# Performance work log

Measured on AMD Instinct MI355X. Metric: run time of the kernel, lower is better.

## Reference

```python
import jax, jax.numpy as jnp
import numpy as np
from math import sqrt

L, H, D, HD, F, V, P = 8, 16, 1024, 64, 4096, 32000, 2048
B, S = 2, 2048
EPS = 1e-5


def _ln(x, g, b):
    m = jnp.mean(x, axis=-1, keepdims=True)
    v = jnp.mean((x - m) ** 2, axis=-1, keepdims=True)
    return (x - m) * jax.lax.rsqrt(v + EPS) * g + b


def setup_inputs() -> dict:
    key = jax.random.key(0)
    ks = jax.random.split(key, 12)
    w = 0.02
    return {
        'input_ids': jax.random.randint(ks[0], (B, S), 0, V),
        'tok_emb': jax.random.normal(ks[1], (V, D), jnp.float32) * w,
        'pos_emb': jax.random.normal(ks[2], (P, D), jnp.float32) * w,
        'emb_g': jnp.ones((D,), jnp.float32),
        'emb_b': jnp.zeros((D,), jnp.float32),
        'ln1_g': jnp.ones((L, D), jnp.float32),
        'ln1_b': jnp.zeros((L, D), jnp.float32),
        'ln2_g': jnp.ones((L, D), jnp.float32),
        'ln2_b': jnp.zeros((L, D), jnp.float32),
        'Wq': jax.random.normal(ks[3], (L, H, D, HD), jnp.float32) * w,
        'bq': jnp.zeros((L, H, HD), jnp.float32),
        'Wk': jax.random.normal(ks[4], (L, H, D, HD), jnp.float32) * w,
        'bk': jnp.zeros((L, H, HD), jnp.float32),
        'Wv': jax.random.normal(ks[5], (L, H, D, HD), jnp.float32) * w,
        'bv': jnp.zeros((L, H, HD), jnp.float32),
        'Wo': jax.random.normal(ks[6], (L, D, D), jnp.float32) * w,
        'bo': jnp.zeros((L, D), jnp.float32),
        'W1': jax.random.normal(ks[7], (L, D, F), jnp.float32) * w,
        'b1': jnp.zeros((L, F), jnp.float32),
        'W2': jax.random.normal(ks[8], (L, F, D), jnp.float32) * w,
        'b2': jnp.zeros((L, D), jnp.float32),
    }


def _encoder(input_ids, tok_emb, pos_emb, emb_g, emb_b, ln1_g, ln1_b, ln2_g,
             ln2_b, Wq, bq, Wk, bk, Wv, bv, Wo, bo, W1, b1, W2, b2):
    seq = input_ids.shape[-1]
    x = tok_emb[input_ids] + pos_emb[:seq][None, :, :]  # [B,S,D]
    x = _ln(x, emb_g, emb_b)  # dropout = identity (eval)

    scale = 1.0 / sqrt(HD)

    def layer(x, p):
        (g1, b1_, g2, b2_, wq, bq_, wk, bk_, wv, bv_, wo, bo_, w1, bb1, w2, bb2) = p
        h = _ln(x, g1, b1_)
        q = jnp.einsum('bsd,hdk->bhsk', h, wq) + bq_[:, None, :]
        k = jnp.einsum('bsd,hdk->bhsk', h, wk) + bk_[:, None, :]
        v = jnp.einsum('bsd,hdk->bhsk', h, wv) + bv_[:, None, :]
        scores = jnp.einsum('bhsk,bhtk->bhst', q, k) * scale
        w = jax.nn.softmax(scores, axis=-1)
        av = jnp.einsum('bhst,bhtk->bhsk', w, v)  # [B,H,S,hd]
        av = jnp.transpose(av, (0, 2, 1, 3)).reshape(x.shape[0], x.shape[1], D)
        x = x + jnp.einsum('bsd,de->bse', av, wo) + bo_
        h2 = _ln(x, g2, b2_)
        f = jax.nn.gelu(jnp.einsum('bsd,df->bsf', h2, w1) + bb1, approximate=False)
        x = x + jnp.einsum('bsf,fd->bsd', f, w2) + bb2
        return x, None

    xs = (ln1_g, ln1_b, ln2_g, ln2_b, Wq, bq, Wk, bk, Wv, bv, Wo, bo, W1, b1, W2, b2)
    x, _ = jax.lax.scan(layer, x, xs)
    return x


def reference(input_ids, tok_emb, pos_emb, emb_g, emb_b, ln1_g, ln1_b, ln2_g,
              ln2_b, Wq, bq, Wk, bk, Wv, bv, Wo, bo, W1, b1, W2, b2):
    return _encoder(input_ids, tok_emb, pos_emb, emb_g, emb_b, ln1_g, ln1_b,
                    ln2_g, ln2_b, Wq, bq, Wk, bk, Wv, bv, Wo, bo, W1, b1, W2, b2)
```

## Files before the change

### kernel.cpp

```cpp
#include <hip/hip_runtime.h>
#include <hip/hip_bf16.h>

#define L_ 8
#define H_ 16
#define D_ 1024
#define HD_ 64
#define F_ 4096
#define B_ 2
#define S_ 2048
#define NTOK (B_*S_)

typedef unsigned short u16;
typedef __bf16 bf16x8 __attribute__((ext_vector_type(8)));
typedef float f32x4 __attribute__((ext_vector_type(4)));

__device__ __forceinline__ u16 f2b(float f){ union{float f; unsigned u;} c; c.f = f; unsigned u = c.u; return (u16)((u + 0x7fffu + ((u>>16)&1u)) >> 16); }
__device__ __forceinline__ u16 f2b_fast(float f){ union{float f; unsigned u;} c; c.f = f; return (u16)((c.u + 0x8000u) >> 16); }
__device__ __forceinline__ float b2f(u16 x){ union{unsigned u; float f;} c; c.u = ((unsigned)x)<<16; return c.f; }

__device__ __forceinline__ void gload16(const u16* g, u16* l){
  __builtin_amdgcn_global_load_lds(
      (const __attribute__((address_space(1))) void*)g,
      (__attribute__((address_space(3))) void*)l,
      16 , 0 , 0 );
}

#define WAITV_BAR(n) do { \
  asm volatile("s_waitcnt vmcnt(%0)" :: "i"(n) : "memory"); \
  __builtin_amdgcn_sched_barrier(0); \
  __builtin_amdgcn_s_barrier(); \
} while(0)

__device__ __forceinline__ void blk_reduce2(float& a, float& b, float* sm){
  for (int off=32; off>0; off>>=1){ a += __shfl_down(a,off); b += __shfl_down(b,off); }
  int w = threadIdx.x>>6, ln = threadIdx.x&63;
  if (ln==0){ sm[w]=a; sm[4+w]=b; }
  __syncthreads();
  a = sm[0]+sm[1]+sm[2]+sm[3];
  b = sm[4]+sm[5]+sm[6]+sm[7];
}

__global__ __launch_bounds__(256) void embed_ln(const int* __restrict__ ids,
    const float* __restrict__ tok, const float* __restrict__ pos,
    const float* __restrict__ g, const float* __restrict__ bb,
    float* __restrict__ x)
{
  __shared__ float sm[8];
  int row = blockIdx.x;
  int s   = row % S_;
  int id  = ids[row];
  const float* te = tok + (size_t)id * D_;
  const float* pe = pos + (size_t)s  * D_;
  float v[4]; float sum=0.f, sq=0.f;
  #pragma unroll
  for (int i=0;i<4;i++){ int d = threadIdx.x + i*256; v[i] = te[d] + pe[d]; sum += v[i]; sq += v[i]*v[i]; }
  blk_reduce2(sum, sq, sm);
  float mean = sum * (1.0f/D_);
  float var  = sq  * (1.0f/D_) - mean*mean;
  float inv  = rsqrtf(var + 1e-5f);
  #pragma unroll
  for (int i=0;i<4;i++){ int d = threadIdx.x + i*256; x[(size_t)row*D_ + d] = (v[i]-mean)*inv*g[d] + bb[d]; }
}

__global__ __launch_bounds__(256) void ln_f32_bf16(const float* __restrict__ x,
    const float* __restrict__ g, const float* __restrict__ bb, u16* __restrict__ out)
{
  __shared__ float sm[8];
  int row = blockIdx.x;
  const float* xr = x + (size_t)row*D_;
  float v[4]; float sum=0.f, sq=0.f;
  #pragma unroll
  for (int i=0;i<4;i++){ int d = threadIdx.x + i*256; v[i] = xr[d]; sum += v[i]; sq += v[i]*v[i]; }
  blk_reduce2(sum, sq, sm);
  float mean = sum * (1.0f/D_);
  float var  = sq  * (1.0f/D_) - mean*mean;
  float inv  = rsqrtf(var + 1e-5f);
  #pragma unroll
  for (int i=0;i<4;i++){ int d = threadIdx.x + i*256; out[(size_t)row*D_ + d] = f2b((v[i]-mean)*inv*g[d] + bb[d]); }
}

__global__ __launch_bounds__(256) void transpose_w(const float* __restrict__ src,
    u16* __restrict__ dst, int R, int C)
{
  __shared__ u16 tile[32][33];
  int c0 = blockIdx.x*32, r0 = blockIdx.y*32;
  int tx = threadIdx.x, ty = threadIdx.y;
  #pragma unroll
  for (int i=0;i<4;i++){
    int r = ty + i*8;
    tile[r][tx] = f2b(src[(size_t)(r0+r)*C + c0 + tx]);
  }
  __syncthreads();
  #pragma unroll
  for (int i=0;i<4;i++){
    int c = ty + i*8;
    dst[(size_t)(c0+c)*R + r0 + tx] = tile[tx][c];
  }
}

__global__ __launch_bounds__(256) void qkv_repack(const float* __restrict__ Wq,
    const float* __restrict__ Wk, const float* __restrict__ Wv,
    u16* __restrict__ dst, int layer)
{
  __shared__ u16 tile[32][33];
  int z = blockIdx.z; int which = z >> 4, h = z & 15;
  const float* W = (which==0) ? Wq : (which==1) ? Wk : Wv;
  const float* src = W + ((size_t)(layer*H_ + h))*D_*HD_;
  int d0 = blockIdx.x*32, c0 = blockIdx.y*32;
  int tx = threadIdx.x, ty = threadIdx.y;
  #pragma unroll
  for (int i=0;i<4;i++){
    int r = ty + i*8;
    tile[r][tx] = f2b(src[(size_t)(d0+r)*HD_ + c0 + tx]);
  }
  __syncthreads();
  #pragma unroll
  for (int i=0;i<4;i++){
    int hd = c0 + ty + i*8;
    dst[(size_t)(which*1024 + h*64 + hd)*D_ + d0 + tx] = tile[tx][ty + i*8];
  }
}

__global__ __launch_bounds__(256) void v_transpose(const u16* __restrict__ qkv, u16* __restrict__ vT)
{
  __shared__ u16 tile[64*64];
  const int tt = blockIdx.x;
  const int bh = blockIdx.y;
  const int b = bh>>4, h = bh&15;
  const int t = threadIdx.x;
  const u16* src = qkv + (size_t)(b*S_ + tt*64)*3072 + 2048 + h*64;
  #pragma unroll
  for (int i=0;i<2;i++){
    int idx = t + i*256;
    int tl = idx>>3, hc = idx&7;
    uint4 v = *(const uint4*)(src + (size_t)tl*3072 + hc*8);
    *(uint4*)(&tile[tl*64 + ((hc ^ (tl&7))<<3)]) = v;
  }
  __syncthreads();
  u16* dst = vT + ((size_t)bh*64)*S_ + tt*64;
  #pragma unroll
  for (int i=0;i<2;i++){
    int idx = t + i*256;
    int hd = idx>>3, tc = idx&7;
    u16 tmp[8];
    #pragma unroll
    for (int j=0;j<8;j++){
      int tk = tc*8 + j;
      tmp[j] = tile[tk*64 + (hd ^ ((tk&7)<<3))];
    }
    *(uint4*)(dst + (size_t)hd*S_ + tc*8) = *(uint4*)tmp;
  }
}

__device__ __forceinline__ void epi_store(float v0,float v1,float v2,float v3,
    float* xres, u16* obf, size_t idx, int epi)
{
  if (epi==1){
    float4 t = *(float4*)(xres + idx);
    t.x += v0; t.y += v1; t.z += v2; t.w += v3;
    *(float4*)(xres + idx) = t;
  } else {
    if (epi==2){
      #define GELU_T(v) { float t2=(v)*(v); float u=(v)*fmaf(t2,0.044715f,1.0f); \
                          float e=exp2f(u*-2.3022082f); (v)=(v)*__builtin_amdgcn_rcpf(1.0f+e); }
      GELU_T(v0); GELU_T(v1); GELU_T(v2); GELU_T(v3);
      #undef GELU_T
    }
    uint2 w;
    w.x = (unsigned)f2b_fast(v0) | ((unsigned)f2b_fast(v1) << 16);
    w.y = (unsigned)f2b_fast(v2) | ((unsigned)f2b_fast(v3) << 16);
    *(uint2*)(obf + idx) = w;
  }
}

__global__ __launch_bounds__(256) void gemm_bf16(
    const u16* __restrict__ A, const u16* __restrict__ Bt,
    const float* __restrict__ bias0, const float* __restrict__ bias1, const float* __restrict__ bias2,
    float* __restrict__ xres, u16* __restrict__ obf,
    int M, int N, int K, int epi)
{
  __shared__ u16 As[128*64];
  __shared__ u16 Bs[128*64];
  const int tid = threadIdx.x;
  const int nbx = gridDim.x;
  const int nwg = nbx * gridDim.y;
  int bid = blockIdx.x + nbx*blockIdx.y;
  int nid = (bid & 7)*(nwg >> 3) + (bid >> 3);
  const int bm = (nid % nbx) * 128;
  const int bn = (nid / nbx) * 128;
  const int wv = tid>>6, ln = tid&63;
  const int wr = wv>>1, wc = wv&1;
  const int l15 = ln&15, lhi = ln>>4;
  const int l8 = ln>>3;
  const int c8s = (ln&7) ^ l8;
  f32x4 acc[4][4];
  const f32x4 zero4 = {0.f,0.f,0.f,0.f};
  #pragma unroll
  for (int i=0;i<4;i++)
    #pragma unroll
    for (int j=0;j<4;j++) acc[i][j] = zero4;

  for (int k0 = 0; k0 < K; k0 += 64) {
    #pragma unroll
    for (int i=0;i<4;i++){
      int row = wv*8 + i*32 + l8;
      gload16(A  + (size_t)(bm+row)*K + k0 + c8s*8, &As[(wv*8 + i*32)*64]);
      gload16(Bt + (size_t)(bn+row)*K + k0 + c8s*8, &Bs[(wv*8 + i*32)*64]);
    }
    __syncthreads();
    #pragma unroll
    for (int ks=0; ks<2; ks++){
      bf16x8 af[4], bfr[4];
      #pragma unroll
      for (int i=0;i<4;i++){
        int ra = wr*64 + i*16 + l15;
        af[i]  = *(const bf16x8*)(&As[ra*64 + (((ks*4+lhi) ^ (ra&7))<<3)]);
        int rb = wc*64 + i*16 + l15;
        bfr[i] = *(const bf16x8*)(&Bs[rb*64 + (((ks*4+lhi) ^ (rb&7))<<3)]);
      }
      #pragma unroll
      for (int i=0;i<4;i++)
        #pragma unroll
        for (int j=0;j<4;j++)
          acc[i][j] = __builtin_amdgcn_mfma_f32_16x16x32_bf16(bfr[j], af[i], acc[i][j], 0,0,0);
    }
    __syncthreads();
  }

  #pragma unroll
  for (int j=0;j<4;j++){
    int col0 = bn + wc*64 + j*16 + lhi*4;
    float4 bv4;
    if (bias1){
      const float* bp = (col0 < 1024) ? (bias0 + col0)
                      : (col0 < 2048) ? (bias1 + col0 - 1024)
                                      : (bias2 + col0 - 2048);
      bv4 = *(const float4*)bp;
    } else {
      bv4 = *(const float4*)(bias0 + col0);
    }
    #pragma unroll
    for (int i=0;i<4;i++){
      int row = bm + wr*64 + i*16 + l15;
      epi_store(acc[i][j][0]+bv4.x, acc[i][j][1]+bv4.y, acc[i][j][2]+bv4.z, acc[i][j][3]+bv4.w,
                xres, obf, (size_t)row*N + col0, epi);
    }
  }
}

__global__ __launch_bounds__(512,2) void gemm256(
    const u16* __restrict__ A, const u16* __restrict__ Bt,
    const float* __restrict__ bias0, const float* __restrict__ bias1, const float* __restrict__ bias2,
    float* __restrict__ xres, u16* __restrict__ obf,
    int M, int N, int K, int epi)
{
  __shared__ u16 As[2][256*64];
  __shared__ u16 Bs[2][256*64];
  const int tid = threadIdx.x;
  const int nbx = gridDim.x;
  const int nwg = nbx * gridDim.y;
  int bid = blockIdx.x + nbx*blockIdx.y;
  int nid = (bid & 7)*(nwg >> 3) + (bid >> 3);
  const int bm = (nid % nbx) * 256;
  const int bn = (nid / nbx) * 256;
  const int wv = tid>>6, ln = tid&63;
  const int wm = wv>>2, wn = wv&3;
  const int l15 = ln&15, lhi = ln>>4;
  const int l8 = ln>>3;
  const int c8s = (ln&7) ^ l8;

  f32x4 acc[2][2][4][2];
  const f32x4 zero4 = {0.f,0.f,0.f,0.f};
  #pragma unroll
  for (int a=0;a<2;a++)
    #pragma unroll
    for (int b=0;b<2;b++)
      #pragma unroll
      for (int i=0;i<4;i++)
        #pragma unroll
        for (int j=0;j<2;j++) acc[a][b][i][j] = zero4;

  const u16* aB0 = A  + (size_t)(bm + wv*16 + l8)*K + c8s*8;
  const u16* bB0 = Bt + (size_t)(bn + wv*16 + l8)*K + c8s*8;

  #define ISSUE(c, kt) do {                                                  \
    const u16* aB = aB0 + (size_t)(kt)*64;                                   \
    const u16* bB = bB0 + (size_t)(kt)*64;                                   \
    gload16(aB,                 &As[c][(wv*16      )*64]);                   \
    gload16(aB + (size_t)8*K,   &As[c][(wv*16 +   8)*64]);                   \
    gload16(bB,                 &Bs[c][(wv*16      )*64]);                   \
    gload16(bB + (size_t)8*K,   &Bs[c][(wv*16 +   8)*64]);                   \
    gload16(bB + (size_t)128*K, &Bs[c][(128 + wv*16    )*64]);               \
    gload16(bB + (size_t)136*K, &Bs[c][(128 + wv*16 + 8)*64]);               \
    gload16(aB + (size_t)128*K, &As[c][(128 + wv*16    )*64]);               \
    gload16(aB + (size_t)136*K, &As[c][(128 + wv*16 + 8)*64]);               \
  } while(0)

  #define READ_B(c) do {                                                     \
    _Pragma("unroll")                                                        \
    for (int qc=0;qc<2;qc++)                                                 \
      _Pragma("unroll")                                                      \
      for (int j=0;j<2;j++){                                                 \
        int rb = qc*128 + wn*32 + j*16 + l15;                                \
        _Pragma("unroll")                                                    \
        for (int ks=0;ks<2;ks++)                                             \
          bfr[qc][j][ks] = *(const bf16x8*)(&Bs[c][rb*64 + (((ks*4+lhi) ^ (rb&7))<<3)]); \
      }                                                                      \
  } while(0)

  #define READ_A(c, qr) do {                                                 \
    _Pragma("unroll")                                                        \
    for (int i=0;i<4;i++){                                                   \
      int ra = (qr)*128 + wm*64 + i*16 + l15;                                \
      _Pragma("unroll")                                                      \
      for (int ks=0;ks<2;ks++)                                               \
        af[i][ks] = *(const bf16x8*)(&As[c][ra*64 + (((ks*4+lhi) ^ (ra&7))<<3)]); \
    }                                                                        \
  } while(0)

  #define MFMA_Q(qr) do {                                                    \
    __builtin_amdgcn_s_setprio(1);                                           \
    _Pragma("unroll")                                                        \
    for (int ks=0;ks<2;ks++)                                                 \
      _Pragma("unroll")                                                      \
      for (int i=0;i<4;i++)                                                  \
        _Pragma("unroll")                                                    \
        for (int qc=0;qc<2;qc++)                                             \
          _Pragma("unroll")                                                  \
          for (int j=0;j<2;j++)                                              \
            acc[qr][qc][i][j] = __builtin_amdgcn_mfma_f32_16x16x32_bf16(     \
                bfr[qc][j][ks], af[i][ks], acc[qr][qc][i][j], 0,0,0);        \
    __builtin_amdgcn_s_setprio(0);                                           \
  } while(0)

  const int nt = K >> 6;
  ISSUE(0, 0);
  WAITV_BAR(2);
  for (int t=0; t<nt-1; ++t){
    int c = t&1;
    ISSUE(c^1, t+1);
    bf16x8 bfr[2][2][2], af[4][2];
    READ_B(c);
    READ_A(c, 0);
    MFMA_Q(0);
    WAITV_BAR(8);
    READ_A(c, 1);
    MFMA_Q(1);
    WAITV_BAR(2);
  }
  {
    int c = (nt-1)&1;
    bf16x8 bfr[2][2][2], af[4][2];
    READ_B(c);
    READ_A(c, 0);
    MFMA_Q(0);
    WAITV_BAR(0);
    READ_A(c, 1);
    MFMA_Q(1);
  }
  #undef ISSUE
  #undef READ_B
  #undef READ_A
  #undef MFMA_Q

  #pragma unroll
  for (int qc=0; qc<2; qc++)
    #pragma unroll
    for (int j=0;j<2;j++){
      int col0 = bn + qc*128 + wn*32 + j*16 + lhi*4;
      float4 bv4;
      if (bias1){
        const float* bp = (col0 < 1024) ? (bias0 + col0)
                        : (col0 < 2048) ? (bias1 + col0 - 1024)
                                        : (bias2 + col0 - 2048);
        bv4 = *(const float4*)bp;
      } else {
        bv4 = *(const float4*)(bias0 + col0);
      }
      #pragma unroll
      for (int qr=0; qr<2; qr++)
        #pragma unroll
        for (int i=0;i<4;i++){
          int row = bm + qr*128 + wm*64 + i*16 + l15;
          epi_store(acc[qr][qc][i][j][0]+bv4.x, acc[qr][qc][i][j][1]+bv4.y,
                    acc[qr][qc][i][j][2]+bv4.z, acc[qr][qc][i][j][3]+bv4.w,
                    xres, obf, (size_t)row*N + col0, epi);
        }
    }
}

__global__ __launch_bounds__(256) void attn_fwd(const u16* __restrict__ qkv,
    const u16* __restrict__ vT, u16* __restrict__ att)
{
  __shared__ u16 Ks[2][64*64];
  __shared__ u16 Vs[2][64*64];
  const int tid = threadIdx.x, wv = tid>>6, ln = tid&63, l15 = ln&15, lhi = ln>>4;
  const int l8 = ln>>3;
  const int cs = (ln&7) ^ l8;
  int bid = blockIdx.x + 32*(blockIdx.y + 16*blockIdx.z);
  int nid = (bid & 7)*128 + (bid >> 3);
  const int qt = nid & 31, h = (nid >> 5) & 15, b = nid >> 9;
  const u16* qg = qkv + (size_t)b*S_*3072 + h*64;
  const u16* kg = qg + 1024;
  const u16* vtg = vT + ((size_t)(b*16 + h)*64)*S_;

  bf16x8 qf[2];
  {
    const u16* qrow = qg + (size_t)(qt*64 + wv*16 + l15)*3072;
    u16 tmp[16];
    *(uint4*)(tmp)   = *(const uint4*)(qrow + lhi*8);
    *(uint4*)(tmp+8) = *(const uint4*)(qrow + 32 + lhi*8);
    #pragma unroll
    for (int i=0;i<16;i++) tmp[i] = f2b_fast(b2f(tmp[i]) * 0.18033688f);
    qf[0] = *(const bf16x8*)(tmp);
    qf[1] = *(const bf16x8*)(tmp+8);
  }
  const f32x4 zero4 = {0.f,0.f,0.f,0.f};
  f32x4 oacc[4];
  #pragma unroll
  for (int j=0;j<4;j++) oacc[j] = zero4;
  float lsum = 0.f;

  #define STAGE_KV(bufi, kti) do {                                            \
    _Pragma("unroll")                                                         \
    for (int i_=0;i_<2;i_++){                                                 \
      int r0_ = wv*8 + i_*32;                                                 \
      int row_ = r0_ + l8;                                                    \
      gload16(kg  + (size_t)((kti)*64+row_)*3072 + cs*8, &Ks[bufi][r0_*64]);  \
      gload16(vtg + (size_t)row_*S_ + (kti)*64 + cs*8,   &Vs[bufi][r0_*64]);  \
    }                                                                         \
  } while(0)

  STAGE_KV(0, 0);
  __syncthreads();
  int buf = 0;

  for (int kt=0; kt<S_/64; kt++){
    if (kt+1 < S_/64) STAGE_KV(buf^1, kt+1);

    f32x4 s[4];
    __builtin_amdgcn_s_setprio(1);
    #pragma unroll
    for (int j=0;j<4;j++){
      s[j] = zero4;
      #pragma unroll
      for (int ks=0; ks<2; ks++){
        int kr = j*16 + l15;
        bf16x8 kf = *(const bf16x8*)(&Ks[buf][kr*64 + (((ks*4+lhi) ^ (kr&7))<<3)]);
        s[j] = __builtin_amdgcn_mfma_f32_16x16x32_bf16(kf, qf[ks], s[j], 0,0,0);
      }
    }
    __builtin_amdgcn_s_setprio(0);

    unsigned pk[8];
    float part = 0.f;
    #pragma unroll
    for (int j=0;j<4;j++){
      float p0 = exp2f(s[j][0]);
      float p1 = exp2f(s[j][1]);
      float p2 = exp2f(s[j][2]);
      float p3 = exp2f(s[j][3]);
      part += (p0+p1)+(p2+p3);
      asm("v_cvt_pk_bf16_f32 %0, %1, %2" : "=v"(pk[j*2])   : "v"(p0), "v"(p1));
      asm("v_cvt_pk_bf16_f32 %0, %1, %2" : "=v"(pk[j*2+1]) : "v"(p2), "v"(p3));
    }
    lsum += part;

    unsigned pw[2][4];
    #pragma unroll
    for (int ks=0; ks<2; ks++){
      #pragma unroll
      for (int w=0; w<4; w++){
        int src = l15 + (lhi&1)*32 + (w>>1)*16;
        unsigned a  = __shfl(pk[ks*4 + (w&1)],     src);
        unsigned bb = __shfl(pk[ks*4 + 2 + (w&1)], src);
        pw[ks][w] = (lhi & 2) ? bb : a;
      }
    }
    bf16x8 pf[2];
    #pragma unroll
    for (int ks=0; ks<2; ks++){
      union { unsigned u[4]; bf16x8 v; } pu;
      pu.u[0]=pw[ks][0]; pu.u[1]=pw[ks][1]; pu.u[2]=pw[ks][2]; pu.u[3]=pw[ks][3];
      pf[ks] = pu.v;
    }

    __builtin_amdgcn_s_setprio(1);
    #pragma unroll
    for (int dj=0; dj<4; dj++){
      #pragma unroll
      for (int ks=0; ks<2; ks++){
        int vr = dj*16 + l15;
        bf16x8 vf = *(const bf16x8*)(&Vs[buf][vr*64 + (((ks*4+lhi) ^ (vr&7))<<3)]);
        oacc[dj] = __builtin_amdgcn_mfma_f32_16x16x32_bf16(pf[ks], vf, oacc[dj], 0,0,0);
      }
    }
    __builtin_amdgcn_s_setprio(0);
    __syncthreads();
    buf ^= 1;
  }
  #undef STAGE_KV

  float tot = lsum + __shfl_xor(lsum, 16);
  tot += __shfl_xor(tot, 32);
  float inv[4];
  #pragma unroll
  for (int r=0;r<4;r++) inv[r] = __builtin_amdgcn_rcpf(__shfl(tot, lhi*4+r));

  #pragma unroll
  for (int dj=0; dj<4; dj++){
    #pragma unroll
    for (int r=0;r<4;r++){
      int q = lhi*4 + r;
      int token = qt*64 + wv*16 + q;
      att[(size_t)(b*S_ + token)*D_ + h*HD_ + dj*16 + l15] = f2b_fast(oacc[dj][r] * inv[r]);
    }
  }
}

extern "C" void kernel_launch(void* const* d_in, const int* in_sizes, int n_in,
                              void* d_out, int out_size, void* d_ws, size_t ws_size,
                              hipStream_t stream)
{
  const int*   ids   = (const int*)d_in[0];
  const float* tok   = (const float*)d_in[1];
  const float* pos   = (const float*)d_in[2];
  const float* emb_g = (const float*)d_in[3];
  const float* emb_b = (const float*)d_in[4];
  const float* ln1g  = (const float*)d_in[5];
  const float* ln1b  = (const float*)d_in[6];
  const float* ln2g  = (const float*)d_in[7];
  const float* ln2b  = (const float*)d_in[8];
  const float* Wq = (const float*)d_in[9];
  const float* bq = (const float*)d_in[10];
  const float* Wk = (const float*)d_in[11];
  const float* bk = (const float*)d_in[12];
  const float* Wv = (const float*)d_in[13];
  const float* bv = (const float*)d_in[14];
  const float* Wo = (const float*)d_in[15];
  const float* bo = (const float*)d_in[16];
  const float* W1 = (const float*)d_in[17];
  const float* b1 = (const float*)d_in[18];
  const float* W2 = (const float*)d_in[19];
  const float* b2 = (const float*)d_in[20];

  float* x = (float*)d_out;
  char* ws = (char*)d_ws;
  u16* h     = (u16*)(ws);
  u16* qkvb  = (u16*)(ws + 8388608);
  u16* att   = (u16*)(ws + 33554432);
  u16* fbuf  = (u16*)(ws + 41943040);
  u16* vT    = fbuf;
  u16* wqkvt = (u16*)(ws + 75497472);
  u16* wot   = (u16*)(ws + 81788928);
  u16* w1t   = (u16*)(ws + 83886080);
  u16* w2t   = (u16*)(ws + 92274688);

  embed_ln<<<NTOK, 256, 0, stream>>>(ids, tok, pos, emb_g, emb_b, x);

  for (int l=0; l<L_; l++){
    ln_f32_bf16<<<NTOK, 256, 0, stream>>>(x, ln1g + l*D_, ln1b + l*D_, h);
    qkv_repack<<<dim3(32,2,48), dim3(32,8), 0, stream>>>(Wq, Wk, Wv, wqkvt, l);
    gemm256<<<dim3(16,12), 512, 0, stream>>>(h, wqkvt,
        bq + l*1024, bk + l*1024, bv + l*1024,
        nullptr, qkvb, NTOK, 3072, 1024, 0);
    v_transpose<<<dim3(32,32), 256, 0, stream>>>(qkvb, vT);
    attn_fwd<<<dim3(S_/64, H_, B_), 256, 0, stream>>>(qkvb, vT, att);
    transpose_w<<<dim3(32,32), dim3(32,8), 0, stream>>>(Wo + (size_t)l*D_*D_, wot, D_, D_);
    gemm_bf16<<<dim3(32,8), 256, 0, stream>>>(att, wot,
        bo + l*D_, nullptr, nullptr,
        x, nullptr, NTOK, 1024, 1024, 1);
    ln_f32_bf16<<<NTOK, 256, 0, stream>>>(x, ln2g + l*D_, ln2b + l*D_, h);
    transpose_w<<<dim3(128,32), dim3(32,8), 0, stream>>>(W1 + (size_t)l*D_*F_, w1t, D_, F_);
    gemm256<<<dim3(16,16), 512, 0, stream>>>(h, w1t,
        b1 + l*F_, nullptr, nullptr,
        nullptr, fbuf, NTOK, 4096, 1024, 2);
    transpose_w<<<dim3(32,128), dim3(32,8), 0, stream>>>(W2 + (size_t)l*F_*D_, w2t, F_, D_);
    gemm_bf16<<<dim3(32,8), 256, 0, stream>>>(fbuf, w2t,
        b2 + l*D_, nullptr, nullptr,
        x, nullptr, NTOK, 1024, 4096, 1);
  }
}
```

Measured before the change: 2.441 ms.

## Process two query tiles per attention wave and vectorize layernorm loads

The attention kernel now handles 128 queries per block, with each wave computing two 16-row query tiles against the same staged K/V tile. Each K and V fragment read from LDS then feeds two MFMAs, and K/V global staging is halved per query. The cost is twice the accumulator registers, which may lower occupancy, and half as many blocks (512). The embedding and layernorm kernels also switch to float4 loads and packed stores.

```diff
diff --git a/kernel.cpp b/kernel.cpp
--- a/kernel.cpp
+++ b/kernel.cpp
@@ -49,17 +49,21 @@
   int row = blockIdx.x;
   int s   = row % S_;
   int id  = ids[row];
-  const float* te = tok + (size_t)id * D_;
-  const float* pe = pos + (size_t)s  * D_;
-  float v[4]; float sum=0.f, sq=0.f;
-  #pragma unroll
-  for (int i=0;i<4;i++){ int d = threadIdx.x + i*256; v[i] = te[d] + pe[d]; sum += v[i]; sq += v[i]*v[i]; }
+  int d0  = threadIdx.x*4;
+  float4 t4 = *(const float4*)(tok + (size_t)id*D_ + d0);
+  float4 p4 = *(const float4*)(pos + (size_t)s *D_ + d0);
+  float4 v; v.x=t4.x+p4.x; v.y=t4.y+p4.y; v.z=t4.z+p4.z; v.w=t4.w+p4.w;
+  float sum = (v.x+v.y)+(v.z+v.w);
+  float sq  = v.x*v.x+v.y*v.y+v.z*v.z+v.w*v.w;
   blk_reduce2(sum, sq, sm);
   float mean = sum * (1.0f/D_);
   float var  = sq  * (1.0f/D_) - mean*mean;
   float inv  = rsqrtf(var + 1e-5f);
-  #pragma unroll
-  for (int i=0;i<4;i++){ int d = threadIdx.x + i*256; x[(size_t)row*D_ + d] = (v[i]-mean)*inv*g[d] + bb[d]; }
+  float4 g4 = *(const float4*)(g + d0);
+  float4 b4 = *(const float4*)(bb + d0);
+  float4 o; o.x=(v.x-mean)*inv*g4.x+b4.x; o.y=(v.y-mean)*inv*g4.y+b4.y;
+            o.z=(v.z-mean)*inv*g4.z+b4.z; o.w=(v.w-mean)*inv*g4.w+b4.w;
+  *(float4*)(x + (size_t)row*D_ + d0) = o;
 }
 
 __global__ __launch_bounds__(256) void ln_f32_bf16(const float* __restrict__ x,
@@ -67,16 +71,20 @@
 {
   __shared__ float sm[8];
   int row = blockIdx.x;
-  const float* xr = x + (size_t)row*D_;
-  float v[4]; float sum=0.f, sq=0.f;
-  #pragma unroll
-  for (int i=0;i<4;i++){ int d = threadIdx.x + i*256; v[i] = xr[d]; sum += v[i]; sq += v[i]*v[i]; }
+  int d0  = threadIdx.x*4;
+  float4 v = *(const float4*)(x + (size_t)row*D_ + d0);
+  float sum = (v.x+v.y)+(v.z+v.w);
+  float sq  = v.x*v.x+v.y*v.y+v.z*v.z+v.w*v.w;
   blk_reduce2(sum, sq, sm);
   float mean = sum * (1.0f/D_);
   float var  = sq  * (1.0f/D_) - mean*mean;
   float inv  = rsqrtf(var + 1e-5f);
-  #pragma unroll
-  for (int i=0;i<4;i++){ int d = threadIdx.x + i*256; out[(size_t)row*D_ + d] = f2b((v[i]-mean)*inv*g[d] + bb[d]); }
+  float4 g4 = *(const float4*)(g + d0);
+  float4 b4 = *(const float4*)(bb + d0);
+  uint2 w;
+  w.x = (unsigned)f2b((v.x-mean)*inv*g4.x+b4.x) | ((unsigned)f2b((v.y-mean)*inv*g4.y+b4.y)<<16);
+  w.y = (unsigned)f2b((v.z-mean)*inv*g4.z+b4.z) | ((unsigned)f2b((v.w-mean)*inv*g4.w+b4.w)<<16);
+  *(uint2*)(out + (size_t)row*D_ + d0) = w;
 }
 
 __global__ __launch_bounds__(256) void transpose_w(const float* __restrict__ src,
@@ -397,29 +405,33 @@
   const int tid = threadIdx.x, wv = tid>>6, ln = tid&63, l15 = ln&15, lhi = ln>>4;
   const int l8 = ln>>3;
   const int cs = (ln&7) ^ l8;
-  int bid = blockIdx.x + 32*(blockIdx.y + 16*blockIdx.z);
-  int nid = (bid & 7)*128 + (bid >> 3);
-  const int qt = nid & 31, h = (nid >> 5) & 15, b = nid >> 9;
+  int bid = blockIdx.x + 16*(blockIdx.y + 16*blockIdx.z);
+  int nid = (bid & 7)*64 + (bid >> 3);
+  const int qt = nid & 15, h = (nid >> 4) & 15, b = nid >> 8;
   const u16* qg = qkv + (size_t)b*S_*3072 + h*64;
   const u16* kg = qg + 1024;
   const u16* vtg = vT + ((size_t)(b*16 + h)*64)*S_;
 
-  bf16x8 qf[2];
+  bf16x8 qfA[2], qfB[2];
   {
-    const u16* qrow = qg + (size_t)(qt*64 + wv*16 + l15)*3072;
-    u16 tmp[16];
-    *(uint4*)(tmp)   = *(const uint4*)(qrow + lhi*8);
-    *(uint4*)(tmp+8) = *(const uint4*)(qrow + 32 + lhi*8);
-    #pragma unroll
-    for (int i=0;i<16;i++) tmp[i] = f2b_fast(b2f(tmp[i]) * 0.18033688f);
-    qf[0] = *(const bf16x8*)(tmp);
-    qf[1] = *(const bf16x8*)(tmp+8);
+    const u16* qrA = qg + (size_t)(qt*128 + wv*32 + l15)*3072;
+    const u16* qrB = qrA + (size_t)16*3072;
+    u16 ta[16], tb[16];
+    *(uint4*)(ta)   = *(const uint4*)(qrA + lhi*8);
+    *(uint4*)(ta+8) = *(const uint4*)(qrA + 32 + lhi*8);
+    *(uint4*)(tb)   = *(const uint4*)(qrB + lhi*8);
+    *(uint4*)(tb+8) = *(const uint4*)(qrB + 32 + lhi*8);
+    #pragma unroll
+    for (int i=0;i<16;i++){ ta[i] = f2b_fast(b2f(ta[i]) * 0.18033688f);
+                            tb[i] = f2b_fast(b2f(tb[i]) * 0.18033688f); }
+    qfA[0] = *(const bf16x8*)(ta); qfA[1] = *(const bf16x8*)(ta+8);
+    qfB[0] = *(const bf16x8*)(tb); qfB[1] = *(const bf16x8*)(tb+8);
   }
   const f32x4 zero4 = {0.f,0.f,0.f,0.f};
-  f32x4 oacc[4];
-  #pragma unroll
-  for (int j=0;j<4;j++) oacc[j] = zero4;
-  float lsum = 0.f;
+  f32x4 oaccA[4], oaccB[4];
+  #pragma unroll
+  for (int j=0;j<4;j++){ oaccA[j] = zero4; oaccB[j] = zero4; }
+  float lsumA = 0.f, lsumB = 0.f;
 
   #define STAGE_KV(bufi, kti) do {                                            \
     _Pragma("unroll")                                                         \
@@ -431,6 +443,23 @@
     }                                                                         \
   } while(0)
 
+  #define EXCHANGE(pk, pf) do {                                               \
+    _Pragma("unroll")                                                         \
+    for (int ks=0; ks<2; ks++){                                               \
+      unsigned pw[4];                                                         \
+      _Pragma("unroll")                                                       \
+      for (int w=0; w<4; w++){                                                \
+        int src = l15 + (lhi&1)*32 + (w>>1)*16;                               \
+        unsigned a  = __shfl(pk[ks*4 + (w&1)],     src);                      \
+        unsigned bb2 = __shfl(pk[ks*4 + 2 + (w&1)], src);                     \
+        pw[w] = (lhi & 2) ? bb2 : a;                                          \
+      }                                                                       \
+      union { unsigned u[4]; bf16x8 v; } pu;                                  \
+      pu.u[0]=pw[0]; pu.u[1]=pw[1]; pu.u[2]=pw[2]; pu.u[3]=pw[3];             \
+      pf[ks] = pu.v;                                                          \
+    }                                                                         \
+  } while(0)
+
   STAGE_KV(0, 0);
   __syncthreads();
   int buf = 0;
@@ -438,52 +467,39 @@
   for (int kt=0; kt<S_/64; kt++){
     if (kt+1 < S_/64) STAGE_KV(buf^1, kt+1);
 
-    f32x4 s[4];
+    f32x4 sA[4], sB[4];
     __builtin_amdgcn_s_setprio(1);
     #pragma unroll
     for (int j=0;j<4;j++){
-      s[j] = zero4;
+      sA[j] = zero4; sB[j] = zero4;
       #pragma unroll
       for (int ks=0; ks<2; ks++){
         int kr = j*16 + l15;
         bf16x8 kf = *(const bf16x8*)(&Ks[buf][kr*64 + (((ks*4+lhi) ^ (kr&7))<<3)]);
-        s[j] = __builtin_amdgcn_mfma_f32_16x16x32_bf16(kf, qf[ks], s[j], 0,0,0);
+        sA[j] = __builtin_amdgcn_mfma_f32_16x16x32_bf16(kf, qfA[ks], sA[j], 0,0,0);
+        sB[j] = __builtin_amdgcn_mfma_f32_16x16x32_bf16(kf, qfB[ks], sB[j], 0,0,0);
       }
     }
     __builtin_amdgcn_s_setprio(0);
 
-    unsigned pk[8];
-    float part = 0.f;
+    unsigned pkA[8], pkB[8];
+    float partA = 0.f, partB = 0.f;
     #pragma unroll
     for (int j=0;j<4;j++){
-      float p0 = exp2f(s[j][0]);
-      float p1 = exp2f(s[j][1]);
-      float p2 = exp2f(s[j][2]);
-      float p3 = exp2f(s[j][3]);
-      part += (p0+p1)+(p2+p3);
-      asm("v_cvt_pk_bf16_f32 %0, %1, %2" : "=v"(pk[j*2])   : "v"(p0), "v"(p1));
-      asm("v_cvt_pk_bf16_f32 %0, %1, %2" : "=v"(pk[j*2+1]) : "v"(p2), "v"(p3));
-    }
-    lsum += part;
-
-    unsigned pw[2][4];
-    #pragma unroll
-    for (int ks=0; ks<2; ks++){
-      #pragma unroll
-      for (int w=0; w<4; w++){
-        int src = l15 + (lhi&1)*32 + (w>>1)*16;
-        unsigned a  = __shfl(pk[ks*4 + (w&1)],     src);
-        unsigned bb = __shfl(pk[ks*4 + 2 + (w&1)], src);
-        pw[ks][w] = (lhi & 2) ? bb : a;
-      }
-    }
-    bf16x8 pf[2];
-    #pragma unroll
-    for (int ks=0; ks<2; ks++){
-      union { unsigned u[4]; bf16x8 v; } pu;
-      pu.u[0]=pw[ks][0]; pu.u[1]=pw[ks][1]; pu.u[2]=pw[ks][2]; pu.u[3]=pw[ks][3];
-      pf[ks] = pu.v;
-    }
+      float a0 = exp2f(sA[j][0]), a1 = exp2f(sA[j][1]), a2 = exp2f(sA[j][2]), a3 = exp2f(sA[j][3]);
+      float b0 = exp2f(sB[j][0]), b1 = exp2f(sB[j][1]), b2 = exp2f(sB[j][2]), b3 = exp2f(sB[j][3]);
+      partA += (a0+a1)+(a2+a3);
+      partB += (b0+b1)+(b2+b3);
+      asm("v_cvt_pk_bf16_f32 %0, %1, %2" : "=v"(pkA[j*2])   : "v"(a0), "v"(a1));
+      asm("v_cvt_pk_bf16_f32 %0, %1, %2" : "=v"(pkA[j*2+1]) : "v"(a2), "v"(a3));
+      asm("v_cvt_pk_bf16_f32 %0, %1, %2" : "=v"(pkB[j*2])   : "v"(b0), "v"(b1));
+      asm("v_cvt_pk_bf16_f32 %0, %1, %2" : "=v"(pkB[j*2+1]) : "v"(b2), "v"(b3));
+    }
+    lsumA += partA; lsumB += partB;
+
+    bf16x8 pfA[2], pfB[2];
+    EXCHANGE(pkA, pfA);
+    EXCHANGE(pkB, pfB);
 
     __builtin_amdgcn_s_setprio(1);
     #pragma unroll
@@ -492,7 +508,8 @@
       for (int ks=0; ks<2; ks++){
         int vr = dj*16 + l15;
         bf16x8 vf = *(const bf16x8*)(&Vs[buf][vr*64 + (((ks*4+lhi) ^ (vr&7))<<3)]);
-        oacc[dj] = __builtin_amdgcn_mfma_f32_16x16x32_bf16(pf[ks], vf, oacc[dj], 0,0,0);
+        oaccA[dj] = __builtin_amdgcn_mfma_f32_16x16x32_bf16(pfA[ks], vf, oaccA[dj], 0,0,0);
+        oaccB[dj] = __builtin_amdgcn_mfma_f32_16x16x32_bf16(pfB[ks], vf, oaccB[dj], 0,0,0);
       }
     }
     __builtin_amdgcn_s_setprio(0);
@@ -500,20 +517,26 @@
     buf ^= 1;
   }
   #undef STAGE_KV
-
-  float tot = lsum + __shfl_xor(lsum, 16);
-  tot += __shfl_xor(tot, 32);
-  float inv[4];
-  #pragma unroll
-  for (int r=0;r<4;r++) inv[r] = __builtin_amdgcn_rcpf(__shfl(tot, lhi*4+r));
+  #undef EXCHANGE
+
+  float totA = lsumA + __shfl_xor(lsumA, 16); totA += __shfl_xor(totA, 32);
+  float totB = lsumB + __shfl_xor(lsumB, 16); totB += __shfl_xor(totB, 32);
+  float invA[4], invB[4];
+  #pragma unroll
+  for (int r=0;r<4;r++){
+    invA[r] = __builtin_amdgcn_rcpf(__shfl(totA, lhi*4+r));
+    invB[r] = __builtin_amdgcn_rcpf(__shfl(totB, lhi*4+r));
+  }
 
   #pragma unroll
   for (int dj=0; dj<4; dj++){
     #pragma unroll
     for (int r=0;r<4;r++){
       int q = lhi*4 + r;
-      int token = qt*64 + wv*16 + q;
-      att[(size_t)(b*S_ + token)*D_ + h*HD_ + dj*16 + l15] = f2b_fast(oacc[dj][r] * inv[r]);
+      int tokA = qt*128 + wv*32 + q;
+      int tokB = tokA + 16;
+      att[(size_t)(b*S_ + tokA)*D_ + h*HD_ + dj*16 + l15] = f2b_fast(oaccA[dj][r] * invA[r]);
+      att[(size_t)(b*S_ + tokB)*D_ + h*HD_ + dj*16 + l15] = f2b_fast(oaccB[dj][r] * invB[r]);
     }
   }
 }
@@ -565,7 +588,7 @@
         bq + l*1024, bk + l*1024, bv + l*1024,
         nullptr, qkvb, NTOK, 3072, 1024, 0);
     v_transpose<<<dim3(32,32), 256, 0, stream>>>(qkvb, vT);
-    attn_fwd<<<dim3(S_/64, H_, B_), 256, 0, stream>>>(qkvb, vT, att);
+    attn_fwd<<<dim3(S_/128, H_, B_), 256, 0, stream>>>(qkvb, vT, att);
     transpose_w<<<dim3(32,32), dim3(32,8), 0, stream>>>(Wo + (size_t)l*D_*D_, wot, D_, D_);
     gemm_bf16<<<dim3(32,8), 256, 0, stream>>>(att, wot,
         bo + l*D_, nullptr, nullptr,
```

Result: no change. 2.422 ms (-0.8%).
